# Performance work log

Measured on AMD Instinct MI355X. Metric: run time of the kernel, lower is better.

## Reference

```python
import jax, jax.numpy as jnp
import numpy as np

EPS = 1e-7
CURVS = (1.0, 0.8, 1.2)
SCALES = (1.0, 0.8, 0.6)


def expmap0(v, c):
    sc = jnp.sqrt(c)
    n = jnp.maximum(jnp.linalg.norm(v, axis=-1, keepdims=True), EPS)
    return jnp.tanh(sc * n) * v / (sc * n)


def projx(x, c):
    max_n = (1.0 - 1e-5) / jnp.sqrt(c)
    n = jnp.maximum(jnp.linalg.norm(x, axis=-1, keepdims=True), EPS)
    return jnp.where(n > max_n, x * (max_n / n), x)


def logmap0(x, c):
    sc = jnp.sqrt(c)
    n = jnp.maximum(jnp.linalg.norm(x, axis=-1, keepdims=True), EPS)
    a = jnp.clip(sc * n, 0.0, 1.0 - 1e-7)
    return jnp.arctanh(a) * x / (sc * n)


def hamilton(q1, q2):
    # q1, q2: [..., 4] (w,x,y,z), broadcasting allowed
    w1, x1, y1, z1 = q1[..., 0], q1[..., 1], q1[..., 2], q1[..., 3]
    w2, x2, y2, z2 = q2[..., 0], q2[..., 1], q2[..., 2], q2[..., 3]
    w = w1 * w2 - x1 * x2 - y1 * y2 - z1 * z2
    x = w1 * x2 + x1 * w2 + y1 * z2 - z1 * y2
    y = w1 * y2 - x1 * z2 + y1 * w2 + z1 * x2
    z = w1 * z2 + x1 * y2 - y1 * x2 + z1 * w2
    return jnp.stack([w, x, y, z], axis=-1)


def mlp(v, Wa, ba, Wb, bb):
    # Linear -> GELU(exact, matching torch default) -> Linear; dropout is eval-mode identity
    return jax.nn.gelu(v @ Wa.T + ba, approximate=False) @ Wb.T + bb


def setup_inputs() -> dict:
    key = jax.random.key(0)
    ks = jax.random.split(key, 24)
    f32 = jnp.float32
    B = 65536
    d = {}
    d['x'] = jax.random.normal(ks[0], (B, 784), dtype=f32)
    # input embedding 784 -> 128, then to level-0 tangent space 128 -> 64
    d['W_in'] = jax.random.normal(ks[1], (128, 784), f32) * (1.0 / np.sqrt(784))
    d['b_in'] = jnp.zeros((128,), f32)
    d['W_tan'] = jax.random.normal(ks[2], (64, 128), f32) * (1.0 / np.sqrt(128))
    d['b_tan'] = jnp.zeros((64,), f32)
    # boundary-manifold tangent points per level (init_scale=0.01 as in BoundaryManifold)
    d['bp0'] = jax.random.normal(ks[3], (5, 64), f32) * 0.01
    d['bp1'] = jax.random.normal(ks[4], (3, 4), f32) * 0.01
    d['bp2'] = jax.random.normal(ks[5], (4, 32), f32) * 0.01
    # rotation 0->1: SO(64) via matrix exponential of a skew-symmetric generator
    d['A_rot'] = jax.random.normal(ks[6], (64, 64), f32) * 0.02
    # rotation 1->2: SO(4) via pvq unit quaternions (std=0.1 init as in source)
    d['p_quat'] = jax.random.normal(ks[7], (4,), f32) * 0.1
    d['q_quat'] = jax.random.normal(ks[8], (4,), f32) * 0.1
    # inter-level MLP transform 0->1: 64 -> 32 -> 4
    d['W0a'] = jax.random.normal(ks[9], (32, 64), f32) * (1.0 / np.sqrt(64))
    d['b0a'] = jnp.zeros((32,), f32)
    d['W0b'] = jax.random.normal(ks[10], (4, 32), f32) * (1.0 / np.sqrt(32))
    d['b0b'] = jnp.zeros((4,), f32)
    # inter-level MLP transform 1->2: 4 -> 16 -> 32
    d['W1a'] = jax.random.normal(ks[11], (16, 4), f32) * (1.0 / np.sqrt(4))
    d['b1a'] = jnp.zeros((16,), f32)
    d['W1b'] = jax.random.normal(ks[12], (32, 16), f32) * (1.0 / np.sqrt(16))
    d['b1b'] = jnp.zeros((32,), f32)
    # output head: concat_tangent (64+4+32=100) -> 10
    d['W_out'] = jax.random.normal(ks[13], (10, 100), f32) * (1.0 / np.sqrt(100))
    d['b_out'] = jnp.zeros((10,), f32)
    return d


def reference(x, W_in, b_in, W_tan, b_tan, bp0, bp1, bp2, A_rot, p_quat, q_quat,
              W0a, b0a, W0b, b0b, W1a, b1a, W1b, b1b, W_out, b_out):
    h = x @ W_in.T + b_in                       # [B, 128]
    v = h @ W_tan.T + b_tan                     # [B, 64] level-0 tangent vector
    bps = (bp0, bp1, bp2)
    level_tangents = []
    carried = None                              # boundary tangent vectors transformed from prev level
    for i in range(3):
        c, s = CURVS[i], SCALES[i]
        # scaled exp/log round trip through the Poincare ball of this level
        x_hyp = projx(expmap0(v * s, c), c)
        v_tan = logmap0(x_hyp, c) / s           # [B, d_i]
        # boundary manifold: tangent -> ball -> proj -> tangent
        b_own = logmap0(projx(expmap0(bps[i], c), c), c)  # [P_i, d_i]
        bnds = b_own if carried is None else jnp.concatenate([b_own, carried], axis=0)
        # relative vectors vs boundary points, mean-aggregated
        rel_agg = v_tan.mean(axis=0, keepdims=False) * 0 + (v_tan[:, None, :] - bnds[None, :, :]).mean(axis=1)  # [B, d_i]
        level_tangents.append(v_tan)
        v_comb = v_tan + rel_agg
        if i == 0:
            R = jax.scipy.linalg.expm(A_rot - A_rot.T)   # SO(64)
            v_rot = v_comb @ R.T
            b_rot = bnds @ R.T
            v = mlp(v_rot, W0a, b0a, W0b, b0b)
            carried = mlp(b_rot, W0a, b0a, W0b, b0b)
        elif i == 1:
            p = p_quat / (jnp.linalg.norm(p_quat) + EPS)
            q = q_quat / (jnp.linalg.norm(q_quat) + EPS)
            v_rot = hamilton(hamilton(p, v_comb), q)     # pvq SO(4) rotation
            b_rot = hamilton(hamilton(p, bnds), q)
            v = mlp(v_rot, W1a, b1a, W1b, b1b)
            carried = mlp(b_rot, W1a, b1a, W1b, b1b)
    agg = jnp.concatenate(level_tangents, axis=-1)       # [B, 100] concat_tangent
    return agg @ W_out.T + b_out                         # [B, 10]
```

## Files before the change

### kernel.cpp

```cpp
#include <hip/hip_runtime.h>
#include <hip/hip_bf16.h>

typedef __attribute__((ext_vector_type(4))) float f32x4;
typedef __attribute__((ext_vector_type(2))) unsigned int u32x2;
typedef __attribute__((ext_vector_type(4))) unsigned int u32x4;
typedef __attribute__((ext_vector_type(8))) short bf16x8;

#define EPSF 1e-7f

__device__ __forceinline__ float radial_factor(float sumsq, float c, float s){
  float sc = sqrtf(c);
  float nv = sqrtf(sumsq);
  float nu = fmaxf(s*nv, EPSF);
  float th = tanhf(sc*nu);
  float r1 = th/sc;
  float maxn = (1.0f - 1e-5f)/sc;
  float r2 = fminf(r1, maxn);
  float n1 = fmaxf(r2, EPSF);
  float a  = fminf(sc*n1, 1.0f - 1e-7f);
  float r3 = 0.5f*logf((1.0f + a)/(1.0f - a));
  return r3*r2/(sc*n1*nu);
}

__device__ __forceinline__ float gelu_f(float x){
  return 0.5f*x*(1.0f + erff(x*0.70710678118654752f));
}

__device__ __forceinline__ unsigned f2bf1(float f){
  unsigned u = __float_as_uint(f);
  return (u + 0x7FFFu + ((u>>16)&1u)) >> 16;
}
__device__ __forceinline__ unsigned f2bf_pk(float lo, float hi){
  unsigned ul = f2bf1(lo);
  unsigned uh = __float_as_uint(hi);
  uh = (uh + 0x7FFFu + ((uh>>16)&1u)) & 0xFFFF0000u;
  return ul | uh;
}

__device__ __forceinline__ void gload_lds16(const void* g, void* l){
  __builtin_amdgcn_global_load_lds((const __attribute__((address_space(1))) unsigned int*)g,
                                   (__attribute__((address_space(3))) unsigned int*)l,
                                   16, 0, 0);
}

#define WS_WC     0
#define WS_BCOMB  204800
#define WS_W0AE   205056
#define WS_BROT0  213248
#define WS_BOWN0  214528
#define WS_W0AT   215808
#define WS_MB0    224000
#define WS_MB1    224256
#define WS_W1AE   224272
#define WS_ZERO   224528
#define WS_V      225280

__global__ __launch_bounds__(256) void prep_a(
    const float* __restrict__ W_in, const float* __restrict__ b_in,
    const float* __restrict__ W_tan, const float* __restrict__ b_tan,
    const float* __restrict__ A_rot, const float* __restrict__ W0a,
    const float* __restrict__ bp0,
    unsigned short* __restrict__ Wc, float* __restrict__ bcomb,
    float* __restrict__ W0aE, float* __restrict__ brot0, float* __restrict__ bown0)
{
  __shared__ __align__(16) float Al[64][68];
  __shared__ __align__(16) float ST[64][68];
  const int bid = blockIdx.x, t = threadIdx.x;

  if (bid < 50){
    if (bid == 0 && t < 64){
      float s = b_tan[t];
      for (int j = 0; j < 128; ++j) s += b_in[j]*W_tan[t*128+j];
      bcomb[t] = s;
    }
    const int g4 = bid*256 + t;
    const int n = g4/200, k4 = (g4 - n*200)*4;
    f32x4 s = {0.f,0.f,0.f,0.f};
    if (k4 < 784){
      for (int j = 0; j < 128; ++j){
        float wt = W_tan[n*128+j];
        f32x4 wi = *(const f32x4*)(W_in + j*784 + k4);
        s += wt*wi;
      }
    }
    u32x2 st = { f2bf_pk(s[0], s[1]), f2bf_pk(s[2], s[3]) };
    const int tsl = k4 >> 5;
    const int q   = (k4 >> 3) & 3;
    const int qp  = q ^ ((n >> 1) & 3);
    const int idx = tsl*2048 + n*32 + qp*8 + (k4 & 7);
    *(u32x2*)(Wc + idx) = st;
  } else {
    for (int m = t; m < 4096; m += 256){
      int r = m >> 6, c = m & 63;
      Al[r][c] = A_rot[m];
    }
    __syncthreads();
    for (int m = t; m < 4096; m += 256){
      int r = m >> 6, c = m & 63;
      ST[r][c] = Al[c][r] - Al[r][c];
    }
    __syncthreads();
    const int wv = t >> 6, lane = t & 63;
    const int row = (bid - 50)*4 + wv;
    if (row < 37){
      float v, sgn;
      if (row < 32){ v = W0a[row*64 + lane]; sgn = 1.f; }
      else {
        const int r = row - 32;
        float b = bp0[r*64 + lane];
        float ssq = b*b;
        #pragma unroll
        for (int d = 1; d < 64; d <<= 1) ssq += __shfl_xor(ssq, d);
        float fc = radial_factor(ssq, 1.0f, 1.0f);
        v = b*fc;
        bown0[r*64 + lane] = v;
        sgn = -1.f;
      }
      float acc = v;
      for (int k = 1; k <= 12; ++k){
        const float coef = sgn/(float)k;
        float nv = 0.f;
        #pragma unroll
        for (int m = 0; m < 64; m += 4){
          f32x4 s4 = *(const f32x4*)&ST[lane][m];
          nv += __int_as_float(__builtin_amdgcn_readlane(__float_as_int(v), m+0))*s4[0];
          nv += __int_as_float(__builtin_amdgcn_readlane(__float_as_int(v), m+1))*s4[1];
          nv += __int_as_float(__builtin_amdgcn_readlane(__float_as_int(v), m+2))*s4[2];
          nv += __int_as_float(__builtin_amdgcn_readlane(__float_as_int(v), m+3))*s4[3];
        }
        nv *= coef;
        v = nv; acc += nv;
      }
      if (row < 32) W0aE[row*64 + lane] = acc;
      else          brot0[(row-32)*64 + lane] = acc;
    }
  }
}

__global__ __launch_bounds__(256) void prep_small(
    const float* __restrict__ bp1,
    const float* __restrict__ p_quat, const float* __restrict__ q_quat,
    const float* __restrict__ b0a, const float* __restrict__ W0b, const float* __restrict__ b0b,
    const float* __restrict__ W1a,
    const float* __restrict__ W0aE, const float* __restrict__ brot0, const float* __restrict__ bown0,
    float* __restrict__ W0aT, float* __restrict__ mb0, float* __restrict__ mb1,
    float* __restrict__ W1aE, float* __restrict__ zerog)
{
  __shared__ float g[5][32];
  __shared__ float c1[5][4];
  __shared__ float fac1[3];
  __shared__ float Mq[4][4];
  const int t = threadIdx.x;

  for (int i = t; i < 2048; i += 256){
    int o = i >> 6, k = i & 63;
    W0aT[k*32 + o] = W0aE[i];
  }
  if (t >= 240) zerog[t - 240] = 0.f;
  if (t < 64){
    float s = 0.f;
    for (int r = 0; r < 5; ++r) s += bown0[r*64 + t];
    mb0[t] = s * 0.2f;
  }
  if (t < 160){
    int r = t >> 5, o = t & 31;
    float s = b0a[o];
    for (int k = 0; k < 64; ++k) s += brot0[r*64+k]*W0aE[o*64+k];
    g[r][o] = gelu_f(s);
  }
  if (t >= 192 && t < 195){
    int r = t - 192;
    float ssq = 0.f;
    for (int j = 0; j < 4; ++j){ float b = bp1[r*4+j]; ssq += b*b; }
    fac1[r] = radial_factor(ssq, 0.8f, 1.0f);
  }
  if (t == 224){
    float pw=p_quat[0],px=p_quat[1],py=p_quat[2],pz=p_quat[3];
    float n1 = sqrtf(pw*pw+px*px+py*py+pz*pz) + EPSF;
    pw/=n1; px/=n1; py/=n1; pz/=n1;
    float qw=q_quat[0],qx=q_quat[1],qy=q_quat[2],qz=q_quat[3];
    float n2 = sqrtf(qw*qw+qx*qx+qy*qy+qz*qz) + EPSF;
    qw/=n2; qx/=n2; qy/=n2; qz/=n2;
    float Lp[4][4] = {{pw,-px,-py,-pz},{px,pw,-pz,py},{py,pz,pw,-px},{pz,-py,px,pw}};
    float Rq[4][4] = {{qw,-qx,-qy,-qz},{qx,qw,qz,-qy},{qy,-qz,qw,qx},{qz,qy,-qx,qw}};
    #pragma unroll
    for (int i = 0; i < 4; ++i)
      #pragma unroll
      for (int k = 0; k < 4; ++k){
        float s = 0.f;
        #pragma unroll
        for (int m = 0; m < 4; ++m) s += Rq[i][m]*Lp[m][k];
        Mq[i][k] = s;
      }
  }
  __syncthreads();
  if (t < 20){
    int r = t >> 2, o = t & 3;
    float s = b0b[o];
    for (int k = 0; k < 32; ++k) s += g[r][k]*W0b[o*32+k];
    c1[r][o] = s;
  }
  __syncthreads();
  if (t < 4){
    float s = 0.f;
    for (int r = 0; r < 3; ++r) s += bp1[r*4+t]*fac1[r];
    for (int r = 0; r < 5; ++r) s += c1[r][t];
    mb1[t] = s * 0.125f;
  }
  if (t >= 64 && t < 128){
    int i = t - 64, o = i >> 2, kq = i & 3;
    float s = 0.f;
    #pragma unroll
    for (int j = 0; j < 4; ++j) s += W1a[o*4+j]*Mq[j][kq];
    W1aE[o*4+kq] = s;
  }
}

__global__ __launch_bounds__(256, 4) void gemm_v(
    const float* __restrict__ x,
    const unsigned short* __restrict__ Wcs,
    const float* __restrict__ bcomb,
    const float* __restrict__ zerog,
    float* __restrict__ v)
{
  __shared__ __align__(16) char smem[36864];
  char* xsB  = smem;
  char* wcsB = smem + 24576;

  const int tid  = threadIdx.x;
  const int lane = tid & 63;
  const int w    = tid >> 6;
  const int wr   = w >> 1, wc = w & 1;
  const int lr   = lane & 15, lkg = lane >> 4;
  const size_t rowBase = (size_t)blockIdx.x * 64;

  const int row8 = lane >> 3;
  const int qs   = lane & 7;
  const int qoff = qs ^ row8;
  const float* xsrcA = x + (rowBase + (size_t)(8*w     + row8))*784 + qoff*4;
  const float* xsrcB = x + (rowBase + (size_t)(8*(w+4) + row8))*784 + qoff*4;
  const unsigned short* wsrc = Wcs + (16*w + (lane>>2))*32 + (lane&3)*8;

  const int rA0 = wr*32 + lr;
  const int sA0 = (2*lkg)     ^ (lr & 7);
  const int sA1 = (2*lkg + 1) ^ (lr & 7);
  const int offA00 = rA0*128 + sA0*16;
  const int offA01 = rA0*128 + sA1*16;
  const int rB0 = wc*32 + lr;
  const int sB  = lkg ^ ((rB0 >> 1) & 3);
  const int offB0 = rB0*64 + sB*16;

#define STAGE(slab, buf) do{                                                   \
    const int ks_ = (slab)*32;                                                 \
    char* xd_ = xsB  + (buf)*8192;                                             \
    char* wd_ = wcsB + (buf)*4096;                                             \
    const float* sa_ = (ks_ + qoff*4 < 784) ? (xsrcA + ks_) : zerog;           \
    const float* sb_ = (ks_ + qoff*4 < 784) ? (xsrcB + ks_) : zerog;           \
    gload_lds16(sa_, xd_ + w*1024);                                            \
    gload_lds16(sb_, xd_ + (w+4)*1024);                                        \
    gload_lds16(wsrc + (size_t)(slab)*2048, wd_ + w*1024);                     \
  }while(0)

  f32x4 acc00 = {}, acc01 = {}, acc10 = {}, acc11 = {};

#define BODY(tt, VMSTR) do{                                                    \
    asm volatile("s_waitcnt " VMSTR ::: "memory");                             \
    __builtin_amdgcn_sched_barrier(0);                                         \
    __builtin_amdgcn_s_barrier();                                              \
    const int cur_ = (tt) % 3;                                                 \
    const char* xb_ = xsB  + cur_*8192;                                        \
    const char* wb_ = wcsB + cur_*4096;                                        \
    f32x4 a00_ = *(const f32x4*)(xb_ + offA00);                                \
    f32x4 a01_ = *(const f32x4*)(xb_ + offA01);                                \
    f32x4 a10_ = *(const f32x4*)(xb_ + offA00 + 2048);                         \
    f32x4 a11_ = *(const f32x4*)(xb_ + offA01 + 2048);                         \
    bf16x8 b0_ = *(const bf16x8*)(wb_ + offB0);                                \
    bf16x8 b1_ = *(const bf16x8*)(wb_ + offB0 + 1024);                         \
    u32x4 pk0_ = { f2bf_pk(a00_[0],a00_[1]), f2bf_pk(a00_[2],a00_[3]),         \
                   f2bf_pk(a01_[0],a01_[1]), f2bf_pk(a01_[2],a01_[3]) };       \
    u32x4 pk1_ = { f2bf_pk(a10_[0],a10_[1]), f2bf_pk(a10_[2],a10_[3]),         \
                   f2bf_pk(a11_[0],a11_[1]), f2bf_pk(a11_[2],a11_[3]) };       \
    bf16x8 af0_ = __builtin_bit_cast(bf16x8, pk0_);                            \
    bf16x8 af1_ = __builtin_bit_cast(bf16x8, pk1_);                            \
    acc00 = __builtin_amdgcn_mfma_f32_16x16x32_bf16(af0_, b0_, acc00, 0,0,0);  \
    acc01 = __builtin_amdgcn_mfma_f32_16x16x32_bf16(af0_, b1_, acc01, 0,0,0);  \
    acc10 = __builtin_amdgcn_mfma_f32_16x16x32_bf16(af1_, b0_, acc10, 0,0,0);  \
    acc11 = __builtin_amdgcn_mfma_f32_16x16x32_bf16(af1_, b1_, acc11, 0,0,0);  \
    asm volatile("s_waitcnt lgkmcnt(0)" ::: "memory");                         \
    __builtin_amdgcn_sched_barrier(0);                                         \
    __builtin_amdgcn_s_barrier();                                              \
    if ((tt) + 3 < 25) STAGE((tt)+3, cur_);                                    \
  }while(0)

  STAGE(0, 0); STAGE(1, 1); STAGE(2, 2);

  for (int t = 0; t < 23; ++t)
    BODY(t, "vmcnt(6)");
  BODY(23, "vmcnt(3)");
  BODY(24, "vmcnt(0)");

#undef BODY
#undef STAGE

  {
    f32x4 accA[2][2] = { {acc00, acc01}, {acc10, acc11} };
    #pragma unroll
    for (int fj = 0; fj < 2; ++fj){
      const int col = wc*32 + fj*16 + lr;
      const float bc = bcomb[col];
      #pragma unroll
      for (int fi = 0; fi < 2; ++fi){
        const int r0 = wr*32 + fi*16 + lkg*4;
        #pragma unroll
        for (int j = 0; j < 4; ++j)
          v[(rowBase + (size_t)(r0 + j))*64 + col] = accA[fi][fj][j] + bc;
      }
    }
  }
}

__global__ __launch_bounds__(256, 4) void row_phase(
    const float* __restrict__ vg,
    const float* __restrict__ W0aT,
    const float* __restrict__ mb0g, const float* __restrict__ mb1g,
    const float* __restrict__ W1aEg,
    const float* __restrict__ b0a, const float* __restrict__ W0b, const float* __restrict__ b0b,
    const float* __restrict__ b1a, const float* __restrict__ W1b, const float* __restrict__ b1b,
    const float* __restrict__ Wout, const float* __restrict__ bout,
    float* __restrict__ out)
{
  __shared__ __align__(16) char smem[38304];
  float* vlds   = (float*)smem;
  float* gv     = (float*)(smem + 19456);
  float* cW0aTS = (float*)(smem + 28672);
  float* g1     = (float*)(smem + 28672);
  float* cW1bS  = (float*)(smem + 33792);
  float* cmb0S  = (float*)(smem + 36864);
  float* cW0bS  = (float*)(smem + 37120);
  float* cW1aES = (float*)(smem + 37632);
  float* cb0aS  = (float*)(smem + 37888);
  float* cb0bS  = (float*)(smem + 38016);
  float* cmb1S  = (float*)(smem + 38032);
  float* cb1aS  = (float*)(smem + 38048);
  float* cb1bS  = (float*)(smem + 38112);
  float* cboutS = (float*)(smem + 38240);

  const int tid = threadIdx.x;
  const size_t rowBase = (size_t)blockIdx.x * 64;

  for (int i = tid; i < 1024; i += 256){
    const int r = i >> 4, seg = i & 15;
    *(f32x4*)&vlds[r*76 + seg*4] = *(const f32x4*)(vg + (rowBase + (size_t)r)*64 + seg*4);
  }
  for (int i = tid; i < 2048; i += 256) cW0aTS[i] = W0aT[i];
  if (tid < 64)  cmb0S[tid] = mb0g[tid];
  if (tid < 32)  cb0aS[tid] = b0a[tid];
  if (tid < 128) cW0bS[tid] = W0b[tid];
  if (tid < 4)   { cb0bS[tid] = b0b[tid]; cmb1S[tid] = mb1g[tid]; }
  if (tid < 64)  cW1aES[tid] = W1aEg[tid];
  if (tid < 16)  cb1aS[tid] = b1a[tid];
  if (tid < 32)  cb1bS[tid] = b1b[tid];
  if (tid < 10)  cboutS[tid] = bout[tid];
  __syncthreads();

  const int row = tid >> 2, p4 = tid & 3;

  {
    f32x4 rv[4];
    float* vptr = &vlds[row*76 + p4*16];
    #pragma unroll
    for (int i = 0; i < 4; ++i) rv[i] = ((const f32x4*)vptr)[i];
    float ssq = 0.f;
    #pragma unroll
    for (int i = 0; i < 4; ++i)
      ssq += rv[i][0]*rv[i][0] + rv[i][1]*rv[i][1] + rv[i][2]*rv[i][2] + rv[i][3]*rv[i][3];
    ssq += __shfl_xor(ssq, 1); ssq += __shfl_xor(ssq, 2);
    const float fac = radial_factor(ssq, 1.0f, 1.0f);
    #pragma unroll
    for (int i = 0; i < 4; ++i){ rv[i] *= fac; ((f32x4*)vptr)[i] = rv[i]; }
  }
  __syncthreads();

  {
    const int og = p4;
    float a0o[8];
    #pragma unroll
    for (int j = 0; j < 8; ++j) a0o[j] = cb0aS[og*8 + j];
    #pragma unroll 4
    for (int k = 0; k < 64; k += 4){
      f32x4 vtv = *(const f32x4*)&vlds[row*76 + k];
      f32x4 mm  = *(const f32x4*)&cmb0S[k];
      #pragma unroll
      for (int u = 0; u < 4; ++u){
        const float vc = 2.f*vtv[u] - mm[u];
        const f32x4* wp = (const f32x4*)&cW0aTS[(k+u)*32 + og*8];
        f32x4 w0 = wp[0], w1 = wp[1];
        #pragma unroll
        for (int j = 0; j < 4; ++j){ a0o[j] += w0[j]*vc; a0o[4+j] += w1[j]*vc; }
      }
    }
    #pragma unroll
    for (int j = 0; j < 8; ++j) gv[row*36 + og*8 + j] = gelu_f(a0o[j]);
  }
  __syncthreads();

  {
    const int o1 = p4;
    float a1 = cb0bS[o1];
    #pragma unroll
    for (int k = 0; k < 32; k += 4){
      f32x4 gg = *(const f32x4*)&gv[row*36 + k];
      f32x4 ww = *(const f32x4*)&cW0bS[o1*32 + k];
      a1 += gg[0]*ww[0] + gg[1]*ww[1] + gg[2]*ww[2] + gg[3]*ww[3];
    }
    float ss1 = a1*a1;
    ss1 += __shfl_xor(ss1, 1); ss1 += __shfl_xor(ss1, 2);
    const float f1v = radial_factor(ss1, 0.8f, 0.8f);
    const float vt1 = a1*f1v;
    vlds[row*76 + 64 + o1] = vt1;
    vlds[row*76 + 68 + o1] = 2.f*vt1 - cmb1S[o1];
  }
  __syncthreads();

  for (int i = tid; i < 512; i += 256) cW1bS[i] = W1b[i];
  {
    const f32x4 vc1 = *(const f32x4*)&vlds[row*76 + 68];
    #pragma unroll
    for (int j = 0; j < 4; ++j){
      const int o = p4*4 + j;
      float s1 = cb1aS[o] + cW1aES[o*4+0]*vc1[0] + cW1aES[o*4+1]*vc1[1]
                          + cW1aES[o*4+2]*vc1[2] + cW1aES[o*4+3]*vc1[3];
      g1[row*20 + o] = gelu_f(s1);
    }
  }
  __syncthreads();

  {
    float v2[8]; float ss2 = 0.f;
    #pragma unroll
    for (int j = 0; j < 8; ++j){
      const int o = p4*8 + j;
      float s = cb1bS[o];
      #pragma unroll
      for (int k = 0; k < 16; k += 4){
        f32x4 gg = *(const f32x4*)&g1[row*20 + k];
        f32x4 ww = *(const f32x4*)&cW1bS[o*16 + k];
        s += gg[0]*ww[0] + gg[1]*ww[1] + gg[2]*ww[2] + gg[3]*ww[3];
      }
      v2[j] = s; ss2 += s*s;
    }
    ss2 += __shfl_xor(ss2, 1); ss2 += __shfl_xor(ss2, 2);
    const float f2v = radial_factor(ss2, 1.2f, 0.6f);
    #pragma unroll
    for (int j = 0; j < 8; ++j) gv[row*36 + p4*8 + j] = v2[j]*f2v;
  }
  __syncthreads();

  for (int idx = tid; idx < 640; idx += 256){
    const int r6 = idx/10, o = idx - r6*10;
    float s = cboutS[o];
    const float* wrow = Wout + o*100;
    const float* vrow = &vlds[r6*76];
    #pragma unroll 4
    for (int k = 0; k < 68; k += 4){
      f32x4 a = *(const f32x4*)(vrow + k);
      f32x4 b = *(const f32x4*)(wrow + k);
      s += a[0]*b[0] + a[1]*b[1] + a[2]*b[2] + a[3]*b[3];
    }
    const float* v2row = &gv[r6*36];
    #pragma unroll 4
    for (int k = 0; k < 32; k += 4){
      f32x4 a = *(const f32x4*)(v2row + k);
      f32x4 b = *(const f32x4*)(wrow + 68 + k);
      s += a[0]*b[0] + a[1]*b[1] + a[2]*b[2] + a[3]*b[3];
    }
    out[(rowBase + (size_t)r6)*10 + o] = s;
  }
}

extern "C" void kernel_launch(void* const* d_in, const int* in_sizes, int n_in,
                              void* d_out, int out_size, void* d_ws, size_t ws_size,
                              hipStream_t stream)
{
  (void)n_in; (void)out_size; (void)ws_size;
  const float* x      = (const float*)d_in[0];
  const float* W_in   = (const float*)d_in[1];
  const float* b_in   = (const float*)d_in[2];
  const float* W_tan  = (const float*)d_in[3];
  const float* b_tan  = (const float*)d_in[4];
  const float* bp0    = (const float*)d_in[5];
  const float* bp1    = (const float*)d_in[6];
  const float* A_rot  = (const float*)d_in[8];
  const float* p_quat = (const float*)d_in[9];
  const float* q_quat = (const float*)d_in[10];
  const float* W0a    = (const float*)d_in[11];
  const float* b0a    = (const float*)d_in[12];
  const float* W0b    = (const float*)d_in[13];
  const float* b0b    = (const float*)d_in[14];
  const float* W1a    = (const float*)d_in[15];
  const float* b1a    = (const float*)d_in[16];
  const float* W1b    = (const float*)d_in[17];
  const float* b1b    = (const float*)d_in[18];
  const float* W_out  = (const float*)d_in[19];
  const float* b_out  = (const float*)d_in[20];

  char* ws = (char*)d_ws;
  unsigned short* Wcs = (unsigned short*)(ws + WS_WC);
  float* bcomb = (float*)(ws + WS_BCOMB);
  float* W0aE  = (float*)(ws + WS_W0AE);
  float* brot0 = (float*)(ws + WS_BROT0);
  float* bown0 = (float*)(ws + WS_BOWN0);
  float* W0aT  = (float*)(ws + WS_W0AT);
  float* mb0   = (float*)(ws + WS_MB0);
  float* mb1   = (float*)(ws + WS_MB1);
  float* W1aE  = (float*)(ws + WS_W1AE);
  float* zerog = (float*)(ws + WS_ZERO);
  float* vbuf  = (float*)(ws + WS_V);

  const int Brows = in_sizes[0] / 784;
  const int nblk  = Brows / 64;

  prep_a<<<60, 256, 0, stream>>>(W_in, b_in, W_tan, b_tan, A_rot, W0a, bp0,
                                 Wcs, bcomb, W0aE, brot0, bown0);
  prep_small<<<1, 256, 0, stream>>>(bp1, p_quat, q_quat, b0a, W0b, b0b, W1a,
                                    W0aE, brot0, bown0, W0aT, mb0, mb1, W1aE, zerog);
  gemm_v<<<nblk, 256, 0, stream>>>(x, Wcs, bcomb, zerog, vbuf);
  row_phase<<<nblk, 256, 0, stream>>>(vbuf, W0aT, mb0, mb1, W1aE,
                                      b0a, W0b, b0b, b1a, W1b, b1b,
                                      W_out, b_out, (float*)d_out);
}
```

Before: 88.35 us.

## Fold prep_small into row_phase and tile W_in×W_tan product through LDS

Removes the single-block prep_small launch by recomputing its small derived quantities (W0a transpose, boundary means, quaternion matrix, carried MLP outputs) redundantly in every row_phase block. Separately, the W_tan·W_in weight-fusion in prep_a becomes an LDS-tiled computation over 13 column blocks instead of 50 blocks each streaming from global memory. This saves one kernel launch and serialization point. In exchange, each row_phase block does extra prologue work and adds a barrier.

```diff
diff --git a/kernel.cpp b/kernel.cpp
--- a/kernel.cpp
+++ b/kernel.cpp
@@ -48,10 +48,6 @@
 #define WS_W0AE   205056
 #define WS_BROT0  213248
 #define WS_BOWN0  214528
-#define WS_W0AT   215808
-#define WS_MB0    224000
-#define WS_MB1    224256
-#define WS_W1AE   224272
 #define WS_ZERO   224528
 #define WS_V      225280
 
@@ -61,47 +57,70 @@
     const float* __restrict__ A_rot, const float* __restrict__ W0a,
     const float* __restrict__ bp0,
     unsigned short* __restrict__ Wc, float* __restrict__ bcomb,
-    float* __restrict__ W0aE, float* __restrict__ brot0, float* __restrict__ bown0)
+    float* __restrict__ W0aE, float* __restrict__ brot0, float* __restrict__ bown0,
+    float* __restrict__ zerog)
 {
+  __shared__ __align__(16) float Wt[64][132];
+  __shared__ __align__(16) float Wi[128][68];
+  __shared__ float bin[128];
   __shared__ __align__(16) float Al[64][68];
   __shared__ __align__(16) float ST[64][68];
   const int bid = blockIdx.x, t = threadIdx.x;
 
-  if (bid < 50){
-    if (bid == 0 && t < 64){
+  if (bid < 13){
+    const int c = bid;
+    for (int i = t; i < 2048; i += 256){
+      const int n = i >> 5, s4 = i & 31;
+      *(f32x4*)&Wt[n][s4*4] = *(const f32x4*)(W_tan + n*128 + s4*4);
+    }
+    for (int i = t; i < 2048; i += 256){
+      const int j = i >> 4, s4 = i & 15;
+      const int col = c*64 + s4*4;
+      f32x4 v = {0.f,0.f,0.f,0.f};
+      if (col < 784) v = *(const f32x4*)(W_in + j*784 + col);
+      *(f32x4*)&Wi[j][s4*4] = v;
+    }
+    if (c == 0 && t < 128) bin[t] = b_in[t];
+    __syncthreads();
+
+    const int q  = t & 15;
+    const int nb = t >> 4;
+    #pragma unroll
+    for (int i = 0; i < 4; ++i){
+      const int n = nb*4 + i;
+      f32x4 acc = {0.f,0.f,0.f,0.f};
+      #pragma unroll 4
+      for (int j = 0; j < 128; ++j)
+        acc += Wt[n][j] * *(const f32x4*)&Wi[j][q*4];
+      const int k4 = c*64 + q*4;
+      if (k4 < 800){
+        u32x2 st = { f2bf_pk(acc[0], acc[1]), f2bf_pk(acc[2], acc[3]) };
+        const int tsl = k4 >> 5;
+        const int qq  = (k4 >> 3) & 3;
+        const int qp  = qq ^ ((n >> 1) & 3);
+        const int idx = tsl*2048 + n*32 + qp*8 + (k4 & 7);
+        *(u32x2*)(Wc + idx) = st;
+      }
+    }
+    if (c == 0 && t < 64){
       float s = b_tan[t];
-      for (int j = 0; j < 128; ++j) s += b_in[j]*W_tan[t*128+j];
+      for (int j = 0; j < 128; ++j) s += bin[j]*Wt[t][j];
       bcomb[t] = s;
     }
-    const int g4 = bid*256 + t;
-    const int n = g4/200, k4 = (g4 - n*200)*4;
-    f32x4 s = {0.f,0.f,0.f,0.f};
-    if (k4 < 784){
-      for (int j = 0; j < 128; ++j){
-        float wt = W_tan[n*128+j];
-        f32x4 wi = *(const f32x4*)(W_in + j*784 + k4);
-        s += wt*wi;
-      }
-    }
-    u32x2 st = { f2bf_pk(s[0], s[1]), f2bf_pk(s[2], s[3]) };
-    const int tsl = k4 >> 5;
-    const int q   = (k4 >> 3) & 3;
-    const int qp  = q ^ ((n >> 1) & 3);
-    const int idx = tsl*2048 + n*32 + qp*8 + (k4 & 7);
-    *(u32x2*)(Wc + idx) = st;
   } else {
+    if (bid == 13 && t < 16) zerog[t] = 0.f;
     for (int m = t; m < 4096; m += 256){
-      int r = m >> 6, c = m & 63;
-      Al[r][c] = A_rot[m];
+      int r = m >> 6, cc = m & 63;
+      Al[r][cc] = A_rot[m];
     }
     __syncthreads();
     for (int m = t; m < 4096; m += 256){
-      int r = m >> 6, c = m & 63;
-      ST[r][c] = Al[c][r] - Al[r][c];
+      int r = m >> 6, cc = m & 63;
+      ST[r][cc] = Al[cc][r] - Al[r][cc];
     }
     __syncthreads();
     const int wv = t >> 6, lane = t & 63;
-    const int row = (bid - 50)*4 + wv;
+    const int row = (bid - 13)*4 + wv;
     if (row < 37){
       float v, sgn;
       if (row < 32){ v = W0a[row*64 + lane]; sgn = 1.f; }
@@ -134,85 +153,6 @@
       if (row < 32) W0aE[row*64 + lane] = acc;
       else          brot0[(row-32)*64 + lane] = acc;
     }
-  }
-}
-
-__global__ __launch_bounds__(256) void prep_small(
-    const float* __restrict__ bp1,
-    const float* __restrict__ p_quat, const float* __restrict__ q_quat,
-    const float* __restrict__ b0a, const float* __restrict__ W0b, const float* __restrict__ b0b,
-    const float* __restrict__ W1a,
-    const float* __restrict__ W0aE, const float* __restrict__ brot0, const float* __restrict__ bown0,
-    float* __restrict__ W0aT, float* __restrict__ mb0, float* __restrict__ mb1,
-    float* __restrict__ W1aE, float* __restrict__ zerog)
-{
-  __shared__ float g[5][32];
-  __shared__ float c1[5][4];
-  __shared__ float fac1[3];
-  __shared__ float Mq[4][4];
-  const int t = threadIdx.x;
-
-  for (int i = t; i < 2048; i += 256){
-    int o = i >> 6, k = i & 63;
-    W0aT[k*32 + o] = W0aE[i];
-  }
-  if (t >= 240) zerog[t - 240] = 0.f;
-  if (t < 64){
-    float s = 0.f;
-    for (int r = 0; r < 5; ++r) s += bown0[r*64 + t];
-    mb0[t] = s * 0.2f;
-  }
-  if (t < 160){
-    int r = t >> 5, o = t & 31;
-    float s = b0a[o];
-    for (int k = 0; k < 64; ++k) s += brot0[r*64+k]*W0aE[o*64+k];
-    g[r][o] = gelu_f(s);
-  }
-  if (t >= 192 && t < 195){
-    int r = t - 192;
-    float ssq = 0.f;
-    for (int j = 0; j < 4; ++j){ float b = bp1[r*4+j]; ssq += b*b; }
-    fac1[r] = radial_factor(ssq, 0.8f, 1.0f);
-  }
-  if (t == 224){
-    float pw=p_quat[0],px=p_quat[1],py=p_quat[2],pz=p_quat[3];
-    float n1 = sqrtf(pw*pw+px*px+py*py+pz*pz) + EPSF;
-    pw/=n1; px/=n1; py/=n1; pz/=n1;
-    float qw=q_quat[0],qx=q_quat[1],qy=q_quat[2],qz=q_quat[3];
-    float n2 = sqrtf(qw*qw+qx*qx+qy*qy+qz*qz) + EPSF;
-    qw/=n2; qx/=n2; qy/=n2; qz/=n2;
-    float Lp[4][4] = {{pw,-px,-py,-pz},{px,pw,-pz,py},{py,pz,pw,-px},{pz,-py,px,pw}};
-    float Rq[4][4] = {{qw,-qx,-qy,-qz},{qx,qw,qz,-qy},{qy,-qz,qw,qx},{qz,qy,-qx,qw}};
-    #pragma unroll
-    for (int i = 0; i < 4; ++i)
-      #pragma unroll
-      for (int k = 0; k < 4; ++k){
-        float s = 0.f;
-        #pragma unroll
-        for (int m = 0; m < 4; ++m) s += Rq[i][m]*Lp[m][k];
-        Mq[i][k] = s;
-      }
-  }
-  __syncthreads();
-  if (t < 20){
-    int r = t >> 2, o = t & 3;
-    float s = b0b[o];
-    for (int k = 0; k < 32; ++k) s += g[r][k]*W0b[o*32+k];
-    c1[r][o] = s;
-  }
-  __syncthreads();
-  if (t < 4){
-    float s = 0.f;
-    for (int r = 0; r < 3; ++r) s += bp1[r*4+t]*fac1[r];
-    for (int r = 0; r < 5; ++r) s += c1[r][t];
-    mb1[t] = s * 0.125f;
-  }
-  if (t >= 64 && t < 128){
-    int i = t - 64, o = i >> 2, kq = i & 3;
-    float s = 0.f;
-    #pragma unroll
-    for (int j = 0; j < 4; ++j) s += W1a[o*4+j]*Mq[j][kq];
-    W1aE[o*4+kq] = s;
   }
 }
 
@@ -321,20 +261,24 @@
 
 __global__ __launch_bounds__(256, 4) void row_phase(
     const float* __restrict__ vg,
-    const float* __restrict__ W0aT,
-    const float* __restrict__ mb0g, const float* __restrict__ mb1g,
-    const float* __restrict__ W1aEg,
+    const float* __restrict__ W0aE, const float* __restrict__ brot0,
+    const float* __restrict__ bown0,
+    const float* __restrict__ bp1,
+    const float* __restrict__ p_quat, const float* __restrict__ q_quat,
+    const float* __restrict__ W1a,
     const float* __restrict__ b0a, const float* __restrict__ W0b, const float* __restrict__ b0b,
     const float* __restrict__ b1a, const float* __restrict__ W1b, const float* __restrict__ b1b,
     const float* __restrict__ Wout, const float* __restrict__ bout,
     float* __restrict__ out)
 {
-  __shared__ __align__(16) char smem[38304];
+  __shared__ __align__(16) char smem[39168];
   float* vlds   = (float*)smem;
   float* gv     = (float*)(smem + 19456);
+  float* W0aE_t = (float*)(smem + 19456);
   float* cW0aTS = (float*)(smem + 28672);
   float* g1     = (float*)(smem + 28672);
   float* cW1bS  = (float*)(smem + 33792);
+  float* brot_t = (float*)(smem + 33792);
   float* cmb0S  = (float*)(smem + 36864);
   float* cW0bS  = (float*)(smem + 37120);
   float* cW1aES = (float*)(smem + 37632);
@@ -344,6 +288,10 @@
   float* cb1aS  = (float*)(smem + 38048);
   float* cb1bS  = (float*)(smem + 38112);
   float* cboutS = (float*)(smem + 38240);
+  float* gS     = (float*)(smem + 38304);
+  float* c1S    = (float*)(smem + 38944);
+  float* fac1S  = (float*)(smem + 39040);
+  float* MqS    = (float*)(smem + 39056);
 
   const int tid = threadIdx.x;
   const size_t rowBase = (size_t)blockIdx.x * 64;
@@ -352,19 +300,61 @@
     const int r = i >> 4, seg = i & 15;
     *(f32x4*)&vlds[r*76 + seg*4] = *(const f32x4*)(vg + (rowBase + (size_t)r)*64 + seg*4);
   }
-  for (int i = tid; i < 2048; i += 256) cW0aTS[i] = W0aT[i];
-  if (tid < 64)  cmb0S[tid] = mb0g[tid];
+  for (int i = tid; i < 2048; i += 256) W0aE_t[i] = W0aE[i];
+  for (int i = tid; i < 320;  i += 256) brot_t[i] = brot0[i];
+  if (tid < 64){
+    float s = 0.f;
+    #pragma unroll
+    for (int r = 0; r < 5; ++r) s += bown0[r*64 + tid];
+    cmb0S[tid] = s * 0.2f;
+  }
   if (tid < 32)  cb0aS[tid] = b0a[tid];
   if (tid < 128) cW0bS[tid] = W0b[tid];
-  if (tid < 4)   { cb0bS[tid] = b0b[tid]; cmb1S[tid] = mb1g[tid]; }
-  if (tid < 64)  cW1aES[tid] = W1aEg[tid];
+  if (tid < 4)   cb0bS[tid] = b0b[tid];
   if (tid < 16)  cb1aS[tid] = b1a[tid];
   if (tid < 32)  cb1bS[tid] = b1b[tid];
   if (tid < 10)  cboutS[tid] = bout[tid];
-  __syncthreads();
-
+  if (tid >= 192 && tid < 195){
+    const int r = tid - 192;
+    float ssq = 0.f;
+    #pragma unroll
+    for (int j = 0; j < 4; ++j){ float b = bp1[r*4+j]; ssq += b*b; }
+    fac1S[r] = radial_factor(ssq, 0.8f, 1.0f);
+  }
+  if (tid == 224){
+    float pw=p_quat[0],px=p_quat[1],py=p_quat[2],pz=p_quat[3];
+    float n1 = sqrtf(pw*pw+px*px+py*py+pz*pz) + EPSF;
+    pw/=n1; px/=n1; py/=n1; pz/=n1;
+    float qw=q_quat[0],qx=q_quat[1],qy=q_quat[2],qz=q_quat[3];
+    float n2 = sqrtf(qw*qw+qx*qx+qy*qy+qz*qz) + EPSF;
+    qw/=n2; qx/=n2; qy/=n2; qz/=n2;
+    float Lp[4][4] = {{pw,-px,-py,-pz},{px,pw,-pz,py},{py,pz,pw,-px},{pz,-py,px,pw}};
+    float Rq[4][4] = {{qw,-qx,-qy,-qz},{qx,qw,qz,-qy},{qy,-qz,qw,qx},{qz,qy,-qx,qw}};
+    #pragma unroll
+    for (int i = 0; i < 4; ++i)
+      #pragma unroll
+      for (int k = 0; k < 4; ++k){
+        float s = 0.f;
+        #pragma unroll
+        for (int m = 0; m < 4; ++m) s += Rq[i][m]*Lp[m][k];
+        MqS[i*4+k] = s;
+      }
+  }
+  __syncthreads();
+
+  for (int i = tid; i < 2048; i += 256)
+    cW0aTS[(i & 63)*32 + (i >> 6)] = W0aE_t[i];
+  if (tid < 160){
+    const int r = tid >> 5, o = tid & 31;
+    float s = cb0aS[o];
+    for (int k = 0; k < 64; k += 4){
+      f32x4 bb = *(const f32x4*)&brot_t[r*64 + k];
+      f32x4 ww = *(const f32x4*)&W0aE_t[o*64 + k];
+      s += bb[0]*ww[0] + bb[1]*ww[1] + bb[2]*ww[2] + bb[3]*ww[3];
+    }
+    gS[r*32 + o] = gelu_f(s);
+  }
   const int row = tid >> 2, p4 = tid & 3;
-
   {
     f32x4 rv[4];
     float* vptr = &vlds[row*76 + p4*16];
@@ -401,6 +391,29 @@
     }
     #pragma unroll
     for (int j = 0; j < 8; ++j) gv[row*36 + og*8 + j] = gelu_f(a0o[j]);
+  }
+  if (tid < 20){
+    const int r = tid >> 2, o = tid & 3;
+    float s = cb0bS[o];
+    for (int k = 0; k < 32; ++k) s += gS[r*32+k]*cW0bS[o*32+k];
+    c1S[r*4 + o] = s;
+  }
+  if (tid >= 64 && tid < 128){
+    const int i = tid - 64, o = i >> 2, kq = i & 3;
+    float s = 0.f;
+    #pragma unroll
+    for (int j = 0; j < 4; ++j) s += W1a[o*4+j]*MqS[j*4+kq];
+    cW1aES[o*4+kq] = s;
+  }
+  __syncthreads();
+
+  if (tid < 4){
+    float s = 0.f;
+    #pragma unroll
+    for (int r = 0; r < 3; ++r) s += bp1[r*4+tid]*fac1S[r];
+    #pragma unroll
+    for (int r = 0; r < 5; ++r) s += c1S[r*4+tid];
+    cmb1S[tid] = s * 0.125f;
   }
   __syncthreads();
 
@@ -510,22 +523,17 @@
   float* W0aE  = (float*)(ws + WS_W0AE);
   float* brot0 = (float*)(ws + WS_BROT0);
   float* bown0 = (float*)(ws + WS_BOWN0);
-  float* W0aT  = (float*)(ws + WS_W0AT);
-  float* mb0   = (float*)(ws + WS_MB0);
-  float* mb1   = (float*)(ws + WS_MB1);
-  float* W1aE  = (float*)(ws + WS_W1AE);
   float* zerog = (float*)(ws + WS_ZERO);
   float* vbuf  = (float*)(ws + WS_V);
 
   const int Brows = in_sizes[0] / 784;
   const int nblk  = Brows / 64;
 
-  prep_a<<<60, 256, 0, stream>>>(W_in, b_in, W_tan, b_tan, A_rot, W0a, bp0,
-                                 Wcs, bcomb, W0aE, brot0, bown0);
-  prep_small<<<1, 256, 0, stream>>>(bp1, p_quat, q_quat, b0a, W0b, b0b, W1a,
-                                    W0aE, brot0, bown0, W0aT, mb0, mb1, W1aE, zerog);
+  prep_a<<<23, 256, 0, stream>>>(W_in, b_in, W_tan, b_tan, A_rot, W0a, bp0,
+                                 Wcs, bcomb, W0aE, brot0, bown0, zerog);
   gemm_v<<<nblk, 256, 0, stream>>>(x, Wcs, bcomb, zerog, vbuf);
-  row_phase<<<nblk, 256, 0, stream>>>(vbuf, W0aT, mb0, mb1, W1aE,
+  row_phase<<<nblk, 256, 0, stream>>>(vbuf, W0aE, brot0, bown0, bp1,
+                                      p_quat, q_quat, W1a,
                                       b0a, W0b, b0b, b1a, W1b, b1b,
                                       W_out, b_out, (float*)d_out);
 }
```

Measured after the change: 94.38 us. +6.8%, slower.

## Fuse GEMM and row-phase kernels and tile the weight-combine prep in LDS

Applied to the files above, without the earlier changes.

Merges the bf16 GEMM kernel and the per-row manifold/MLP kernel into one. The 64x64 result tile now stays in LDS instead of being written to and re-read from a global workspace, which removes that intermediate round trip and one kernel launch. Separately, the combined W_tan·W_in prep is reorganised into 13 blocks that stage both matrices in LDS, so W_in is not re-read from global memory for every output element. The fused kernel reuses the GEMM's LDS staging area for the row phase, which is a race risk if all waves have not finished the GEMM before the buffer is overwritten.

```diff
diff --git a/kernel.cpp b/kernel.cpp
--- a/kernel.cpp
+++ b/kernel.cpp
@@ -53,7 +53,6 @@
 #define WS_MB1    224256
 #define WS_W1AE   224272
 #define WS_ZERO   224528
-#define WS_V      225280
 
 __global__ __launch_bounds__(256) void prep_a(
     const float* __restrict__ W_in, const float* __restrict__ b_in,
@@ -61,47 +60,70 @@
     const float* __restrict__ A_rot, const float* __restrict__ W0a,
     const float* __restrict__ bp0,
     unsigned short* __restrict__ Wc, float* __restrict__ bcomb,
-    float* __restrict__ W0aE, float* __restrict__ brot0, float* __restrict__ bown0)
+    float* __restrict__ W0aE, float* __restrict__ brot0, float* __restrict__ bown0,
+    float* __restrict__ zerog)
 {
+  __shared__ __align__(16) float Wt[64][132];
+  __shared__ __align__(16) float Wi[128][68];
+  __shared__ float bin[128];
   __shared__ __align__(16) float Al[64][68];
   __shared__ __align__(16) float ST[64][68];
   const int bid = blockIdx.x, t = threadIdx.x;
 
-  if (bid < 50){
-    if (bid == 0 && t < 64){
+  if (bid < 13){
+    const int c = bid;
+    for (int i = t; i < 2048; i += 256){
+      const int n = i >> 5, s4 = i & 31;
+      *(f32x4*)&Wt[n][s4*4] = *(const f32x4*)(W_tan + n*128 + s4*4);
+    }
+    for (int i = t; i < 2048; i += 256){
+      const int j = i >> 4, s4 = i & 15;
+      const int col = c*64 + s4*4;
+      f32x4 v = {0.f,0.f,0.f,0.f};
+      if (col < 784) v = *(const f32x4*)(W_in + j*784 + col);
+      *(f32x4*)&Wi[j][s4*4] = v;
+    }
+    if (c == 0 && t < 128) bin[t] = b_in[t];
+    __syncthreads();
+
+    const int q  = t & 15;
+    const int nb = t >> 4;
+    #pragma unroll
+    for (int i = 0; i < 4; ++i){
+      const int n = nb*4 + i;
+      f32x4 acc = {0.f,0.f,0.f,0.f};
+      #pragma unroll 4
+      for (int j = 0; j < 128; ++j)
+        acc += Wt[n][j] * *(const f32x4*)&Wi[j][q*4];
+      const int k4 = c*64 + q*4;
+      if (k4 < 800){
+        u32x2 st = { f2bf_pk(acc[0], acc[1]), f2bf_pk(acc[2], acc[3]) };
+        const int tsl = k4 >> 5;
+        const int qq  = (k4 >> 3) & 3;
+        const int qp  = qq ^ ((n >> 1) & 3);
+        const int idx = tsl*2048 + n*32 + qp*8 + (k4 & 7);
+        *(u32x2*)(Wc + idx) = st;
+      }
+    }
+    if (c == 0 && t < 64){
       float s = b_tan[t];
-      for (int j = 0; j < 128; ++j) s += b_in[j]*W_tan[t*128+j];
+      for (int j = 0; j < 128; ++j) s += bin[j]*Wt[t][j];
       bcomb[t] = s;
     }
-    const int g4 = bid*256 + t;
-    const int n = g4/200, k4 = (g4 - n*200)*4;
-    f32x4 s = {0.f,0.f,0.f,0.f};
-    if (k4 < 784){
-      for (int j = 0; j < 128; ++j){
-        float wt = W_tan[n*128+j];
-        f32x4 wi = *(const f32x4*)(W_in + j*784 + k4);
-        s += wt*wi;
-      }
-    }
-    u32x2 st = { f2bf_pk(s[0], s[1]), f2bf_pk(s[2], s[3]) };
-    const int tsl = k4 >> 5;
-    const int q   = (k4 >> 3) & 3;
-    const int qp  = q ^ ((n >> 1) & 3);
-    const int idx = tsl*2048 + n*32 + qp*8 + (k4 & 7);
-    *(u32x2*)(Wc + idx) = st;
   } else {
+    if (bid == 13 && t < 16) zerog[t] = 0.f;
     for (int m = t; m < 4096; m += 256){
-      int r = m >> 6, c = m & 63;
-      Al[r][c] = A_rot[m];
+      int r = m >> 6, cc = m & 63;
+      Al[r][cc] = A_rot[m];
     }
     __syncthreads();
     for (int m = t; m < 4096; m += 256){
-      int r = m >> 6, c = m & 63;
-      ST[r][c] = Al[c][r] - Al[r][c];
+      int r = m >> 6, cc = m & 63;
+      ST[r][cc] = Al[cc][r] - Al[r][cc];
     }
     __syncthreads();
     const int wv = t >> 6, lane = t & 63;
-    const int row = (bid - 50)*4 + wv;
+    const int row = (bid - 13)*4 + wv;
     if (row < 37){
       float v, sgn;
       if (row < 32){ v = W0a[row*64 + lane]; sgn = 1.f; }
@@ -144,7 +166,7 @@
     const float* __restrict__ W1a,
     const float* __restrict__ W0aE, const float* __restrict__ brot0, const float* __restrict__ bown0,
     float* __restrict__ W0aT, float* __restrict__ mb0, float* __restrict__ mb1,
-    float* __restrict__ W1aE, float* __restrict__ zerog)
+    float* __restrict__ W1aE)
 {
   __shared__ float g[5][32];
   __shared__ float c1[5][4];
@@ -156,7 +178,6 @@
     int o = i >> 6, k = i & 63;
     W0aT[k*32 + o] = W0aE[i];
   }
-  if (t >= 240) zerog[t - 240] = 0.f;
   if (t < 64){
     float s = 0.f;
     for (int r = 0; r < 5; ++r) s += bown0[r*64 + t];
@@ -216,16 +237,36 @@
   }
 }
 
-__global__ __launch_bounds__(256, 4) void gemm_v(
+__global__ __launch_bounds__(256, 4) void mega_fused(
     const float* __restrict__ x,
     const unsigned short* __restrict__ Wcs,
     const float* __restrict__ bcomb,
     const float* __restrict__ zerog,
-    float* __restrict__ v)
+    const float* __restrict__ W0aT,
+    const float* __restrict__ mb0g, const float* __restrict__ mb1g,
+    const float* __restrict__ W1aEg,
+    const float* __restrict__ b0a, const float* __restrict__ W0b, const float* __restrict__ b0b,
+    const float* __restrict__ b1a, const float* __restrict__ W1b, const float* __restrict__ b1b,
+    const float* __restrict__ Wout, const float* __restrict__ bout,
+    float* __restrict__ out)
 {
-  __shared__ __align__(16) char smem[36864];
-  char* xsB  = smem;
-  char* wcsB = smem + 24576;
+  __shared__ __align__(16) char smem[38304];
+  char* xsB    = smem;
+  char* wcsB   = smem + 24576;
+  float* vlds  = (float*)smem;
+  float* gv    = (float*)(smem + 19456);
+  float* cW0aTS= (float*)(smem + 28672);
+  float* g1    = (float*)(smem + 28672);
+  float* cW1bS = (float*)(smem + 33792);
+  float* cmb0S  = (float*)(smem + 36864);
+  float* cW0bS  = (float*)(smem + 37120);
+  float* cW1aES = (float*)(smem + 37632);
+  float* cb0aS  = (float*)(smem + 37888);
+  float* cb0bS  = (float*)(smem + 38016);
+  float* cmb1S  = (float*)(smem + 38032);
+  float* cb1aS  = (float*)(smem + 38048);
+  float* cb1bS  = (float*)(smem + 38112);
+  float* cboutS = (float*)(smem + 38240);
 
   const int tid  = threadIdx.x;
   const int lane = tid & 63;
@@ -233,6 +274,15 @@
   const int wr   = w >> 1, wc = w & 1;
   const int lr   = lane & 15, lkg = lane >> 4;
   const size_t rowBase = (size_t)blockIdx.x * 64;
+
+  if (tid < 64)  cmb0S[tid] = mb0g[tid];
+  if (tid < 128) cW0bS[tid] = W0b[tid];
+  if (tid < 64)  cW1aES[tid] = W1aEg[tid];
+  if (tid < 32)  cb0aS[tid] = b0a[tid];
+  if (tid < 4)   { cb0bS[tid] = b0b[tid]; cmb1S[tid] = mb1g[tid]; }
+  if (tid < 16)  cb1aS[tid] = b1a[tid];
+  if (tid < 32)  cb1bS[tid] = b1b[tid];
+  if (tid < 10)  cboutS[tid] = bout[tid];
 
   const int row8 = lane >> 3;
   const int qs   = lane & 7;
@@ -313,54 +363,11 @@
         const int r0 = wr*32 + fi*16 + lkg*4;
         #pragma unroll
         for (int j = 0; j < 4; ++j)
-          v[(rowBase + (size_t)(r0 + j))*64 + col] = accA[fi][fj][j] + bc;
-      }
-    }
-  }
-}
-
-__global__ __launch_bounds__(256, 4) void row_phase(
-    const float* __restrict__ vg,
-    const float* __restrict__ W0aT,
-    const float* __restrict__ mb0g, const float* __restrict__ mb1g,
-    const float* __restrict__ W1aEg,
-    const float* __restrict__ b0a, const float* __restrict__ W0b, const float* __restrict__ b0b,
-    const float* __restrict__ b1a, const float* __restrict__ W1b, const float* __restrict__ b1b,
-    const float* __restrict__ Wout, const float* __restrict__ bout,
-    float* __restrict__ out)
-{
-  __shared__ __align__(16) char smem[38304];
-  float* vlds   = (float*)smem;
-  float* gv     = (float*)(smem + 19456);
-  float* cW0aTS = (float*)(smem + 28672);
-  float* g1     = (float*)(smem + 28672);
-  float* cW1bS  = (float*)(smem + 33792);
-  float* cmb0S  = (float*)(smem + 36864);
-  float* cW0bS  = (float*)(smem + 37120);
-  float* cW1aES = (float*)(smem + 37632);
-  float* cb0aS  = (float*)(smem + 37888);
-  float* cb0bS  = (float*)(smem + 38016);
-  float* cmb1S  = (float*)(smem + 38032);
-  float* cb1aS  = (float*)(smem + 38048);
-  float* cb1bS  = (float*)(smem + 38112);
-  float* cboutS = (float*)(smem + 38240);
-
-  const int tid = threadIdx.x;
-  const size_t rowBase = (size_t)blockIdx.x * 64;
-
-  for (int i = tid; i < 1024; i += 256){
-    const int r = i >> 4, seg = i & 15;
-    *(f32x4*)&vlds[r*76 + seg*4] = *(const f32x4*)(vg + (rowBase + (size_t)r)*64 + seg*4);
+          vlds[(r0 + j)*76 + col] = accA[fi][fj][j] + bc;
+      }
+    }
   }
   for (int i = tid; i < 2048; i += 256) cW0aTS[i] = W0aT[i];
-  if (tid < 64)  cmb0S[tid] = mb0g[tid];
-  if (tid < 32)  cb0aS[tid] = b0a[tid];
-  if (tid < 128) cW0bS[tid] = W0b[tid];
-  if (tid < 4)   { cb0bS[tid] = b0b[tid]; cmb1S[tid] = mb1g[tid]; }
-  if (tid < 64)  cW1aES[tid] = W1aEg[tid];
-  if (tid < 16)  cb1aS[tid] = b1a[tid];
-  if (tid < 32)  cb1bS[tid] = b1b[tid];
-  if (tid < 10)  cboutS[tid] = bout[tid];
   __syncthreads();
 
   const int row = tid >> 2, p4 = tid & 3;
@@ -515,17 +522,15 @@
   float* mb1   = (float*)(ws + WS_MB1);
   float* W1aE  = (float*)(ws + WS_W1AE);
   float* zerog = (float*)(ws + WS_ZERO);
-  float* vbuf  = (float*)(ws + WS_V);
 
   const int Brows = in_sizes[0] / 784;
   const int nblk  = Brows / 64;
 
-  prep_a<<<60, 256, 0, stream>>>(W_in, b_in, W_tan, b_tan, A_rot, W0a, bp0,
-                                 Wcs, bcomb, W0aE, brot0, bown0);
+  prep_a<<<23, 256, 0, stream>>>(W_in, b_in, W_tan, b_tan, A_rot, W0a, bp0,
+                                 Wcs, bcomb, W0aE, brot0, bown0, zerog);
   prep_small<<<1, 256, 0, stream>>>(bp1, p_quat, q_quat, b0a, W0b, b0b, W1a,
-                                    W0aE, brot0, bown0, W0aT, mb0, mb1, W1aE, zerog);
-  gemm_v<<<nblk, 256, 0, stream>>>(x, Wcs, bcomb, zerog, vbuf);
-  row_phase<<<nblk, 256, 0, stream>>>(vbuf, W0aT, mb0, mb1, W1aE,
-                                      b0a, W0b, b0b, b1a, W1b, b1b,
-                                      W_out, b_out, (float*)d_out);
-}
+                                    W0aE, brot0, bown0, W0aT, mb0, mb1, W1aE);
+  mega_fused<<<nblk, 256, 0, stream>>>(x, Wcs, bcomb, zerog, W0aT, mb0, mb1, W1aE,
+                                       b0a, W0b, b0b, b1a, W1b, b1b,
+                                       W_out, b_out, (float*)d_out);
+}
```

Measured after the change: 79.39 us. 1.11x faster.
